# Optimization experiments

Measured on AMD Instinct MI355X. Metric: run time of the kernel, lower is better.

The kernel has to match this reference:

```python
import jax, jax.numpy as jnp
import numpy as np

B, S, DM, H = 2, 2048, 512, 8
DH = DM // H


def setup_inputs() -> dict:
    key = jax.random.key(0)
    ks = jax.random.split(key, 20)
    sc = 0.02
    d = {}
    d["q"] = jax.random.normal(ks[0], (B, S, DM), jnp.float32)
    d["k"] = jax.random.normal(ks[1], (B, S, DM), jnp.float32)
    d["v"] = jax.random.normal(ks[2], (B, S, DM), jnp.float32)
    d["xdiff"] = jax.random.normal(ks[3], (B, S, S), jnp.float32)
    d["mask"] = jax.random.randint(ks[4], (B, 1, 1, S), 0, 2, jnp.int32)
    # learned params (keras Dense: kernel + bias)
    d["Wq"] = jax.random.normal(ks[5], (DM, DM), jnp.float32) * sc
    d["bq"] = jnp.zeros((DM,), jnp.float32)
    d["Wk"] = jax.random.normal(ks[6], (DM, DM), jnp.float32) * sc
    d["bk"] = jnp.zeros((DM,), jnp.float32)
    d["Wv"] = jax.random.normal(ks[7], (DM, DM), jnp.float32) * sc
    d["bv"] = jnp.zeros((DM,), jnp.float32)
    d["Wa"] = jax.random.normal(ks[8], (DM, H), jnp.float32) * sc
    d["ba"] = jnp.zeros((H,), jnp.float32)
    d["Wb"] = jax.random.normal(ks[9], (DM, H), jnp.float32) * sc
    d["bb"] = jnp.zeros((H,), jnp.float32)
    d["Wo"] = jax.random.normal(ks[10], (DM, DM), jnp.float32) * sc
    d["bo"] = jnp.zeros((DM,), jnp.float32)
    return d


def reference(q, k, v, xdiff, mask, Wq, bq, Wk, bk, Wv, bv, Wa, ba, Wb, bb, Wo, bo):
    b, s, dm = q.shape
    h, dh = H, DH
    qp = q @ Wq + bq            # [B,S,DM]
    kp = k @ Wk + bk
    vp = v @ Wv + bv
    # per-head alpha/beta from projected q: [B,S,H] -> [B,H,S]
    a = jnp.transpose(qp @ Wa + ba, (0, 2, 1))
    bb_ = jnp.transpose(qp @ Wb + bb, (0, 2, 1))
    # split heads -> [B,H,S,DH]
    qh = qp.reshape(b, s, h, dh).transpose(0, 2, 1, 3)
    kh = kp.reshape(b, s, h, dh).transpose(0, 2, 1, 3)
    vh = vp.reshape(b, s, h, dh).transpose(0, 2, 1, 3)
    logits = jnp.einsum('bhqd,bhkd->bhqk', qh, kh) / jnp.sqrt(jnp.float32(dh))
    logits = logits + mask.astype(jnp.float32) * (-1e9)
    xd = xdiff[:, None]          # [B,1,S,S] broadcast over heads
    logits = logits + a[..., None] * xd + bb_[..., None] * (xd * xd)
    attn = jax.nn.softmax(logits, axis=-1)
    out = jnp.einsum('bhqk,bhkd->bhqd', attn, vh)
    out = out.transpose(0, 2, 1, 3).reshape(b, s, dm)
    return out @ Wo + bo, attn
```

## Files before the change

kernel.cpp:

```cpp
#include <hip/hip_runtime.h>
#include <stdint.h>

#define BB 2
#define SS 2048
#define DMODEL 512
#define NH 8
#define DHD 64

typedef __attribute__((ext_vector_type(8))) short bf16x8;
typedef __attribute__((ext_vector_type(4))) short s16x4;
typedef __attribute__((ext_vector_type(4))) float fx4;

__device__ __forceinline__ short f2bf(float f) {
    union { float f; uint32_t u; } c; c.f = f;
    uint32_t u = c.u;
    u += 0x7fffu + ((u >> 16) & 1u);
    return (short)(u >> 16);
}
__device__ __forceinline__ float bf2f(short s) {
    union { uint32_t u; float f; } c; c.u = ((uint32_t)(uint16_t)s) << 16;
    return c.f;
}

template<int A_BF16, int OUT_BF16>
__global__ __launch_bounds__(256, 4) void gemm_bias_k(
    const void* __restrict__ Ap, const float* __restrict__ W,
    const float* __restrict__ bias, void* __restrict__ Cp)
{
    __shared__ short As[64 * 40];
    __shared__ short Bs[64 * 40];
    const int tid = threadIdx.x;
    const int w = tid >> 6, lane = tid & 63;
    const int cl = lane & 15, quad = lane >> 4;
    const int mi = w >> 1, ni = w & 1;
    const int m0 = blockIdx.x * 64, n0 = blockIdx.y * 64;
    const float* Af = (const float*)Ap;
    const short* Ab = (const short*)Ap;
    fx4 acc[2][2] = {};

    for (int k0 = 0; k0 < DMODEL; k0 += 32) {
#pragma unroll
        for (int it = 0; it < 2; ++it) {
            int idx = tid + it * 256;
            int row = idx >> 3, kq = (idx & 7) * 4;
            s16x4 sv;
            if (A_BF16) {
                sv = *(const s16x4*)&Ab[(size_t)(m0 + row) * DMODEL + k0 + kq];
            } else {
                const float4 vv = *(const float4*)&Af[(size_t)(m0 + row) * DMODEL + k0 + kq];
                sv.x = f2bf(vv.x); sv.y = f2bf(vv.y); sv.z = f2bf(vv.z); sv.w = f2bf(vv.w);
            }
            *(s16x4*)&As[row * 40 + kq] = sv;
        }
#pragma unroll
        for (int it = 0; it < 2; ++it) {
            int idx = tid + it * 256;
            int kk = idx >> 4, nq = (idx & 15) * 4;
            const float4 vv = *(const float4*)&W[(size_t)(k0 + kk) * DMODEL + n0 + nq];
            Bs[(nq + 0) * 40 + kk] = f2bf(vv.x);
            Bs[(nq + 1) * 40 + kk] = f2bf(vv.y);
            Bs[(nq + 2) * 40 + kk] = f2bf(vv.z);
            Bs[(nq + 3) * 40 + kk] = f2bf(vv.w);
        }
        __syncthreads();
        bf16x8 af[2], bfr[2];
#pragma unroll
        for (int i = 0; i < 2; ++i)
            af[i] = *(const bf16x8*)&As[(mi * 32 + i * 16 + cl) * 40 + quad * 8];
#pragma unroll
        for (int j = 0; j < 2; ++j)
            bfr[j] = *(const bf16x8*)&Bs[(ni * 32 + j * 16 + cl) * 40 + quad * 8];
#pragma unroll
        for (int i = 0; i < 2; ++i)
#pragma unroll
            for (int j = 0; j < 2; ++j)
                acc[i][j] = __builtin_amdgcn_mfma_f32_16x16x32_bf16(af[i], bfr[j], acc[i][j], 0, 0, 0);
        __syncthreads();
    }
#pragma unroll
    for (int i = 0; i < 2; ++i) {
#pragma unroll
        for (int j = 0; j < 2; ++j) {
            int col = n0 + ni * 32 + j * 16 + cl;
            float bv = bias[col];
#pragma unroll
            for (int r = 0; r < 4; ++r) {
                int row = m0 + mi * 32 + i * 16 + quad * 4 + r;
                float v = acc[i][j][r] + bv;
                if (OUT_BF16) ((short*)Cp)[(size_t)row * DMODEL + col] = f2bf(v);
                else          ((float*)Cp)[(size_t)row * DMODEL + col] = v;
            }
        }
    }
}

__global__ __launch_bounds__(64) void ab_k(
    const short* __restrict__ qp,
    const float* __restrict__ Wa, const float* __restrict__ ba,
    const float* __restrict__ Wb, const float* __restrict__ bbias,
    float* __restrict__ a_ws, float* __restrict__ b_ws)
{
    const int r = blockIdx.x;
    const int b = r >> 11, s = r & 2047;
    const int lane = threadIdx.x;
    float qv[8];
    s16x4 q0 = *(const s16x4*)&qp[(size_t)r * DMODEL + lane * 8];
    s16x4 q1 = *(const s16x4*)&qp[(size_t)r * DMODEL + lane * 8 + 4];
    qv[0] = bf2f(q0.x); qv[1] = bf2f(q0.y); qv[2] = bf2f(q0.z); qv[3] = bf2f(q0.w);
    qv[4] = bf2f(q1.x); qv[5] = bf2f(q1.y); qv[6] = bf2f(q1.z); qv[7] = bf2f(q1.w);
    float pa[8] = {}, pb[8] = {};
#pragma unroll
    for (int kk = 0; kk < 8; ++kk) {
        int k = lane * 8 + kk;
        const float4 wa0 = *(const float4*)&Wa[k * 8];
        const float4 wa1 = *(const float4*)&Wa[k * 8 + 4];
        const float4 wb0 = *(const float4*)&Wb[k * 8];
        const float4 wb1 = *(const float4*)&Wb[k * 8 + 4];
        float qk = qv[kk];
        pa[0] += qk * wa0.x; pa[1] += qk * wa0.y; pa[2] += qk * wa0.z; pa[3] += qk * wa0.w;
        pa[4] += qk * wa1.x; pa[5] += qk * wa1.y; pa[6] += qk * wa1.z; pa[7] += qk * wa1.w;
        pb[0] += qk * wb0.x; pb[1] += qk * wb0.y; pb[2] += qk * wb0.z; pb[3] += qk * wb0.w;
        pb[4] += qk * wb1.x; pb[5] += qk * wb1.y; pb[6] += qk * wb1.z; pb[7] += qk * wb1.w;
    }
#pragma unroll
    for (int h = 0; h < 8; ++h) {
#pragma unroll
        for (int off = 1; off < 64; off <<= 1) {
            pa[h] += __shfl_xor(pa[h], off);
            pb[h] += __shfl_xor(pb[h], off);
        }
    }
    if (lane == 0) {
#pragma unroll
        for (int h = 0; h < 8; ++h) {
            a_ws[(b * NH + h) * SS + s] = pa[h] + ba[h];
            b_ws[(b * NH + h) * SS + s] = pb[h] + bbias[h];
        }
    }
}

__global__ __launch_bounds__(256, 2) void attn_k(
    const short* __restrict__ qp, const short* __restrict__ kp, const short* __restrict__ vp,
    const float* __restrict__ a_ws, const float* __restrict__ b_ws,
    const float* __restrict__ xdiff, const int* __restrict__ mask,
    float* __restrict__ attn, short* __restrict__ ao)
{
    __shared__ short qs[16 * 72];
    __shared__ short kv[4][64 * 72];
    __shared__ short ps[4][16 * 72];
    __shared__ float redm[64], reds[64], rowa[16], rowb[16];

    const int tid = threadIdx.x;
    const int w = tid >> 6, lane = tid & 63;
    const int cl = lane & 15, quad = lane >> 4;
    const int bh = blockIdx.x;
    const int b = bh >> 3, h = bh & 7;
    const int q0 = blockIdx.y * 16;
    const int bS = b * SS;

    for (int idx = tid; idx < 16 * 64; idx += 256) {
        int i = idx >> 6, k = idx & 63;
        qs[i * 72 + k] = qp[(size_t)(bS + q0 + i) * DMODEL + h * DHD + k];
    }
    if (tid < 16) {
        rowa[tid] = a_ws[(b * NH + h) * SS + q0 + tid];
        rowb[tid] = b_ws[(b * NH + h) * SS + q0 + tid];
    }
    __syncthreads();

    bf16x8 qf[2];
#pragma unroll
    for (int kc = 0; kc < 2; ++kc)
        qf[kc] = *(const bf16x8*)&qs[cl * 72 + kc * 32 + quad * 8];
    float ra[4], rb[4];
#pragma unroll
    for (int r = 0; r < 4; ++r) { ra[r] = rowa[quad * 4 + r]; rb[r] = rowb[quad * 4 + r]; }

    short* kvw = kv[w];
    short* psw = ps[w];
    const int j0w = w * 512;

    fx4 s[8][4];
    float rmax[4] = {-3e38f, -3e38f, -3e38f, -3e38f};

#pragma unroll
    for (int t = 0; t < 8; ++t) {
        const int j0 = j0w + t * 64;
#pragma unroll
        for (int p = 0; p < 16; ++p) {
            int jr = quad + p * 4;
            *(s16x4*)&kvw[jr * 72 + cl * 4] =
                *(const s16x4*)&kp[(size_t)(bS + j0 + jr) * DMODEL + h * DHD + cl * 4];
        }
        fx4 qk[4] = {};
#pragma unroll
        for (int nb = 0; nb < 4; ++nb)
#pragma unroll
            for (int kc = 0; kc < 2; ++kc) {
                bf16x8 kf = *(const bf16x8*)&kvw[(nb * 16 + cl) * 72 + kc * 32 + quad * 8];
                qk[nb] = __builtin_amdgcn_mfma_f32_16x16x32_bf16(qf[kc], kf, qk[nb], 0, 0, 0);
            }
#pragma unroll
        for (int nb = 0; nb < 4; ++nb) {
            const int j = j0 + nb * 16 + cl;
            const float mv = -1.0e9f * (float)mask[bS + j];
#pragma unroll
            for (int r = 0; r < 4; ++r) {
                const int qi = q0 + quad * 4 + r;
                const float xd = xdiff[(size_t)(bS + qi) * SS + j];
                float v = qk[nb][r] * 0.125f + mv + ra[r] * xd + rb[r] * (xd * xd);
                s[t][nb][r] = v;
                rmax[r] = fmaxf(rmax[r], v);
            }
        }
    }

#pragma unroll
    for (int off = 1; off < 16; off <<= 1)
#pragma unroll
        for (int r = 0; r < 4; ++r)
            rmax[r] = fmaxf(rmax[r], __shfl_xor(rmax[r], off));
    if (cl == 0)
#pragma unroll
        for (int r = 0; r < 4; ++r) redm[w * 16 + quad * 4 + r] = rmax[r];
    __syncthreads();
    float gm[4];
#pragma unroll
    for (int r = 0; r < 4; ++r) {
        int i = quad * 4 + r;
        gm[r] = fmaxf(fmaxf(redm[i], redm[16 + i]), fmaxf(redm[32 + i], redm[48 + i]));
    }

    float rsum[4] = {};
#pragma unroll
    for (int t = 0; t < 8; ++t)
#pragma unroll
        for (int nb = 0; nb < 4; ++nb)
#pragma unroll
            for (int r = 0; r < 4; ++r) {
                float e = exp2f((s[t][nb][r] - gm[r]) * 1.44269504f);
                s[t][nb][r] = e;
                rsum[r] += e;
            }
#pragma unroll
    for (int off = 1; off < 16; off <<= 1)
#pragma unroll
        for (int r = 0; r < 4; ++r)
            rsum[r] += __shfl_xor(rsum[r], off);
    if (cl == 0)
#pragma unroll
        for (int r = 0; r < 4; ++r) reds[w * 16 + quad * 4 + r] = rsum[r];
    __syncthreads();
    float gs[4];
#pragma unroll
    for (int r = 0; r < 4; ++r) {
        int i = quad * 4 + r;
        gs[r] = 1.0f / (reds[i] + reds[16 + i] + reds[32 + i] + reds[48 + i]);
    }

    fx4 oacc[4] = {};
    float* attn_bh = attn + (size_t)(b * NH + h) * SS * SS;
#pragma unroll
    for (int t = 0; t < 8; ++t) {
        const int j0 = j0w + t * 64;
#pragma unroll
        for (int p4 = 0; p4 < 16; ++p4) {
            s16x4 tmp;
            tmp.x = vp[(size_t)(bS + j0 + p4 * 4 + 0) * DMODEL + h * DHD + lane];
            tmp.y = vp[(size_t)(bS + j0 + p4 * 4 + 1) * DMODEL + h * DHD + lane];
            tmp.z = vp[(size_t)(bS + j0 + p4 * 4 + 2) * DMODEL + h * DHD + lane];
            tmp.w = vp[(size_t)(bS + j0 + p4 * 4 + 3) * DMODEL + h * DHD + lane];
            *(s16x4*)&kvw[lane * 72 + p4 * 4] = tmp;
        }
#pragma unroll
        for (int nb = 0; nb < 4; ++nb) {
            const int j = j0 + nb * 16 + cl;
#pragma unroll
            for (int r = 0; r < 4; ++r) {
                float p = s[t][nb][r] * gs[r];
                attn_bh[(size_t)(q0 + quad * 4 + r) * SS + j] = p;
                psw[(quad * 4 + r) * 72 + nb * 16 + cl] = f2bf(p);
            }
        }
        bf16x8 pf[2];
#pragma unroll
        for (int kc = 0; kc < 2; ++kc)
            pf[kc] = *(const bf16x8*)&psw[cl * 72 + kc * 32 + quad * 8];
#pragma unroll
        for (int nb = 0; nb < 4; ++nb)
#pragma unroll
            for (int kc = 0; kc < 2; ++kc) {
                bf16x8 vf = *(const bf16x8*)&kvw[(nb * 16 + cl) * 72 + kc * 32 + quad * 8];
                oacc[nb] = __builtin_amdgcn_mfma_f32_16x16x32_bf16(pf[kc], vf, oacc[nb], 0, 0, 0);
            }
    }

    __syncthreads();
    float* ored = (float*)kv;
#pragma unroll
    for (int nb = 0; nb < 4; ++nb)
#pragma unroll
        for (int r = 0; r < 4; ++r)
            ored[w * 1024 + (quad * 4 + r) * 64 + nb * 16 + cl] = oacc[nb][r];
    __syncthreads();
    {
        int i = tid >> 4, dq = (tid & 15) * 4;
        float sx = 0, sy = 0, sz = 0, sw = 0;
#pragma unroll
        for (int ww = 0; ww < 4; ++ww) {
            const float4 vv = *(const float4*)&ored[ww * 1024 + i * 64 + dq];
            sx += vv.x; sy += vv.y; sz += vv.z; sw += vv.w;
        }
        s16x4 o;
        o.x = f2bf(sx); o.y = f2bf(sy); o.z = f2bf(sz); o.w = f2bf(sw);
        *(s16x4*)&ao[(size_t)(bS + q0 + i) * DMODEL + h * DHD + dq] = o;
    }
}

extern "C" void kernel_launch(void* const* d_in, const int* in_sizes, int n_in,
                              void* d_out, int out_size, void* d_ws, size_t ws_size,
                              hipStream_t stream)
{
    (void)in_sizes; (void)n_in; (void)out_size; (void)ws_size;
    const float* q     = (const float*)d_in[0];
    const float* k     = (const float*)d_in[1];
    const float* v     = (const float*)d_in[2];
    const float* xdiff = (const float*)d_in[3];
    const int*   mask  = (const int*)d_in[4];
    const float* Wq = (const float*)d_in[5];
    const float* bq = (const float*)d_in[6];
    const float* Wk = (const float*)d_in[7];
    const float* bk = (const float*)d_in[8];
    const float* Wv = (const float*)d_in[9];
    const float* bv = (const float*)d_in[10];
    const float* Wa = (const float*)d_in[11];
    const float* ba = (const float*)d_in[12];
    const float* Wb = (const float*)d_in[13];
    const float* bb = (const float*)d_in[14];
    const float* Wo = (const float*)d_in[15];
    const float* bo = (const float*)d_in[16];

    char* ws = (char*)d_ws;
    short* qp   = (short*)(ws + 0);
    short* kp   = (short*)(ws + 4194304);
    short* vp   = (short*)(ws + 8388608);
    float* a_ws = (float*)(ws + 12582912);
    float* b_ws = (float*)(ws + 12713984);
    short* ao   = (short*)(ws + 12845056);

    float* out  = (float*)d_out;
    float* attn = out + (size_t)BB * SS * DMODEL;

    dim3 g(64, 8), blk(256);
    hipLaunchKernelGGL((gemm_bias_k<0, 1>), g, blk, 0, stream, q, Wq, bq, qp);
    hipLaunchKernelGGL((gemm_bias_k<0, 1>), g, blk, 0, stream, k, Wk, bk, kp);
    hipLaunchKernelGGL((gemm_bias_k<0, 1>), g, blk, 0, stream, v, Wv, bv, vp);
    hipLaunchKernelGGL(ab_k, dim3(4096), dim3(64), 0, stream, qp, Wa, ba, Wb, bb, a_ws, b_ws);
    hipLaunchKernelGGL(attn_k, dim3(16, 128), dim3(256), 0, stream,
                       qp, kp, vp, a_ws, b_ws, xdiff, mask, attn, ao);
    hipLaunchKernelGGL((gemm_bias_k<1, 0>), g, blk, 0, stream, ao, Wo, bo, out);
}
```

Before: 546.7 us.

## Fuse QKV projections, store V transposed, widen attention to 8 waves

The three input projection GEMMs become one launch over a z-dimension, and the V projection is written transposed as [B, DM, S]. The attention kernel then reads K and transposed V fragments straight from global memory instead of staging them through LDS. It also doubles the block to 512 threads (8 waves, 256 keys each), which halves the per-wave score register array. The cost of the uncoalesced strided V gathers and per-tile LDS copies is meant to go away, in exchange for scattered 8-byte transposed stores in the V GEMM and more reliance on L2 for K/V reuse.

```diff
diff --git a/kernel.cpp b/kernel.cpp
--- a/kernel.cpp
+++ b/kernel.cpp
@@ -22,10 +22,11 @@
     return c.f;
 }
 
-template<int A_BF16, int OUT_BF16>
-__global__ __launch_bounds__(256, 4) void gemm_bias_k(
-    const void* __restrict__ Ap, const float* __restrict__ W,
-    const float* __restrict__ bias, void* __restrict__ Cp)
+__global__ __launch_bounds__(256, 4) void qkv_gemm_k(
+    const float* __restrict__ q, const float* __restrict__ Wq, const float* __restrict__ bq,
+    const float* __restrict__ k, const float* __restrict__ Wk, const float* __restrict__ bk,
+    const float* __restrict__ v, const float* __restrict__ Wv, const float* __restrict__ bv,
+    short* __restrict__ qp, short* __restrict__ kp, short* __restrict__ vt)
 {
     __shared__ short As[64 * 40];
     __shared__ short Bs[64 * 40];
@@ -34,8 +35,10 @@
     const int cl = lane & 15, quad = lane >> 4;
     const int mi = w >> 1, ni = w & 1;
     const int m0 = blockIdx.x * 64, n0 = blockIdx.y * 64;
-    const float* Af = (const float*)Ap;
-    const short* Ab = (const short*)Ap;
+    const int z = blockIdx.z;
+    const float* Af   = (z == 0) ? q  : (z == 1) ? k  : v;
+    const float* W    = (z == 0) ? Wq : (z == 1) ? Wk : Wv;
+    const float* bias = (z == 0) ? bq : (z == 1) ? bk : bv;
     fx4 acc[2][2] = {};
 
     for (int k0 = 0; k0 < DMODEL; k0 += 32) {
@@ -43,13 +46,9 @@
         for (int it = 0; it < 2; ++it) {
             int idx = tid + it * 256;
             int row = idx >> 3, kq = (idx & 7) * 4;
+            const float4 vv = *(const float4*)&Af[(size_t)(m0 + row) * DMODEL + k0 + kq];
             s16x4 sv;
-            if (A_BF16) {
-                sv = *(const s16x4*)&Ab[(size_t)(m0 + row) * DMODEL + k0 + kq];
-            } else {
-                const float4 vv = *(const float4*)&Af[(size_t)(m0 + row) * DMODEL + k0 + kq];
-                sv.x = f2bf(vv.x); sv.y = f2bf(vv.y); sv.z = f2bf(vv.z); sv.w = f2bf(vv.w);
-            }
+            sv.x = f2bf(vv.x); sv.y = f2bf(vv.y); sv.z = f2bf(vv.z); sv.w = f2bf(vv.w);
             *(s16x4*)&As[row * 40 + kq] = sv;
         }
 #pragma unroll
@@ -77,21 +76,89 @@
                 acc[i][j] = __builtin_amdgcn_mfma_f32_16x16x32_bf16(af[i], bfr[j], acc[i][j], 0, 0, 0);
         __syncthreads();
     }
+    short* Cp = (z == 0) ? qp : (z == 1) ? kp : vt;
 #pragma unroll
     for (int i = 0; i < 2; ++i) {
 #pragma unroll
         for (int j = 0; j < 2; ++j) {
             int col = n0 + ni * 32 + j * 16 + cl;
-            float bv = bias[col];
+            float bv4 = bias[col];
+            int rowbase = m0 + mi * 32 + i * 16 + quad * 4;
+            if (z < 2) {
+#pragma unroll
+                for (int r = 0; r < 4; ++r)
+                    Cp[(size_t)(rowbase + r) * DMODEL + col] = f2bf(acc[i][j][r] + bv4);
+            } else {
+                int b = rowbase >> 11, s0 = rowbase & 2047;
+                s16x4 o;
+                o.x = f2bf(acc[i][j][0] + bv4);
+                o.y = f2bf(acc[i][j][1] + bv4);
+                o.z = f2bf(acc[i][j][2] + bv4);
+                o.w = f2bf(acc[i][j][3] + bv4);
+                *(s16x4*)&Cp[((size_t)b * DMODEL + col) * SS + s0] = o;
+            }
+        }
+    }
+}
+
+__global__ __launch_bounds__(256, 4) void out_gemm_k(
+    const short* __restrict__ Ab, const float* __restrict__ W,
+    const float* __restrict__ bias, float* __restrict__ Cp)
+{
+    __shared__ short As[64 * 40];
+    __shared__ short Bs[64 * 40];
+    const int tid = threadIdx.x;
+    const int w = tid >> 6, lane = tid & 63;
+    const int cl = lane & 15, quad = lane >> 4;
+    const int mi = w >> 1, ni = w & 1;
+    const int m0 = blockIdx.x * 64, n0 = blockIdx.y * 64;
+    fx4 acc[2][2] = {};
+
+    for (int k0 = 0; k0 < DMODEL; k0 += 32) {
+#pragma unroll
+        for (int it = 0; it < 2; ++it) {
+            int idx = tid + it * 256;
+            int row = idx >> 3, kq = (idx & 7) * 4;
+            *(s16x4*)&As[row * 40 + kq] =
+                *(const s16x4*)&Ab[(size_t)(m0 + row) * DMODEL + k0 + kq];
+        }
+#pragma unroll
+        for (int it = 0; it < 2; ++it) {
+            int idx = tid + it * 256;
+            int kk = idx >> 4, nq = (idx & 15) * 4;
+            const float4 vv = *(const float4*)&W[(size_t)(k0 + kk) * DMODEL + n0 + nq];
+            Bs[(nq + 0) * 40 + kk] = f2bf(vv.x);
+            Bs[(nq + 1) * 40 + kk] = f2bf(vv.y);
+            Bs[(nq + 2) * 40 + kk] = f2bf(vv.z);
+            Bs[(nq + 3) * 40 + kk] = f2bf(vv.w);
+        }
+        __syncthreads();
+        bf16x8 af[2], bfr[2];
+#pragma unroll
+        for (int i = 0; i < 2; ++i)
+            af[i] = *(const bf16x8*)&As[(mi * 32 + i * 16 + cl) * 40 + quad * 8];
+#pragma unroll
+        for (int j = 0; j < 2; ++j)
+            bfr[j] = *(const bf16x8*)&Bs[(ni * 32 + j * 16 + cl) * 40 + quad * 8];
+#pragma unroll
+        for (int i = 0; i < 2; ++i)
+#pragma unroll
+            for (int j = 0; j < 2; ++j)
+                acc[i][j] = __builtin_amdgcn_mfma_f32_16x16x32_bf16(af[i], bfr[j], acc[i][j], 0, 0, 0);
+        __syncthreads();
+    }
+#pragma unroll
+    for (int i = 0; i < 2; ++i)
+#pragma unroll
+        for (int j = 0; j < 2; ++j) {
+            int col = n0 + ni * 32 + j * 16 + cl;
+            float bv4 = bias[col];
 #pragma unroll
             for (int r = 0; r < 4; ++r) {
                 int row = m0 + mi * 32 + i * 16 + quad * 4 + r;
-                float v = acc[i][j][r] + bv;
-                if (OUT_BF16) ((short*)Cp)[(size_t)row * DMODEL + col] = f2bf(v);
-                else          ((float*)Cp)[(size_t)row * DMODEL + col] = v;
-            }
-        }
-    }
+                Cp[(size_t)row * DMODEL + col] = acc[i][j][r] + bv4;
+            }
+        }
 }
 
 __global__ __launch_bounds__(64) void ab_k(
@@ -101,7 +168,6 @@
     float* __restrict__ a_ws, float* __restrict__ b_ws)
 {
     const int r = blockIdx.x;
-    const int b = r >> 11, s = r & 2047;
     const int lane = threadIdx.x;
     float qv[8];
     s16x4 q0 = *(const s16x4*)&qp[(size_t)r * DMODEL + lane * 8];
@@ -123,14 +189,14 @@
         pb[4] += qk * wb1.x; pb[5] += qk * wb1.y; pb[6] += qk * wb1.z; pb[7] += qk * wb1.w;
     }
 #pragma unroll
-    for (int h = 0; h < 8; ++h) {
+    for (int h = 0; h < 8; ++h)
 #pragma unroll
         for (int off = 1; off < 64; off <<= 1) {
             pa[h] += __shfl_xor(pa[h], off);
             pb[h] += __shfl_xor(pb[h], off);
         }
-    }
     if (lane == 0) {
+        int b = r >> 11, s = r & 2047;
 #pragma unroll
         for (int h = 0; h < 8; ++h) {
             a_ws[(b * NH + h) * SS + s] = pa[h] + ba[h];
@@ -139,16 +205,15 @@
     }
 }
 
-__global__ __launch_bounds__(256, 2) void attn_k(
-    const short* __restrict__ qp, const short* __restrict__ kp, const short* __restrict__ vp,
+__global__ __launch_bounds__(512, 4) void attn_k(
+    const short* __restrict__ qp, const short* __restrict__ kp, const short* __restrict__ vt,
     const float* __restrict__ a_ws, const float* __restrict__ b_ws,
     const float* __restrict__ xdiff, const int* __restrict__ mask,
     float* __restrict__ attn, short* __restrict__ ao)
 {
-    __shared__ short qs[16 * 72];
-    __shared__ short kv[4][64 * 72];
-    __shared__ short ps[4][16 * 72];
-    __shared__ float redm[64], reds[64], rowa[16], rowb[16];
+    __shared__ short ps[8][16 * 72];
+    __shared__ float ored[4][16 * 68];
+    __shared__ float redm[128], reds[128], rowa[16], rowb[16];
 
     const int tid = threadIdx.x;
     const int w = tid >> 6, lane = tid & 63;
@@ -158,59 +223,49 @@
     const int q0 = blockIdx.y * 16;
     const int bS = b * SS;
 
-    for (int idx = tid; idx < 16 * 64; idx += 256) {
-        int i = idx >> 6, k = idx & 63;
-        qs[i * 72 + k] = qp[(size_t)(bS + q0 + i) * DMODEL + h * DHD + k];
-    }
     if (tid < 16) {
-        rowa[tid] = a_ws[(b * NH + h) * SS + q0 + tid];
-        rowb[tid] = b_ws[(b * NH + h) * SS + q0 + tid];
-    }
-    __syncthreads();
-
+        rowa[tid] = a_ws[bh * SS + q0 + tid];
+        rowb[tid] = b_ws[bh * SS + q0 + tid];
+    }
+    __syncthreads();
+
+    const short* qbase = qp + (size_t)(bS + q0 + cl) * DMODEL + h * DHD + quad * 8;
     bf16x8 qf[2];
-#pragma unroll
-    for (int kc = 0; kc < 2; ++kc)
-        qf[kc] = *(const bf16x8*)&qs[cl * 72 + kc * 32 + quad * 8];
+    qf[0] = *(const bf16x8*)(qbase);
+    qf[1] = *(const bf16x8*)(qbase + 32);
+
     float ra[4], rb[4];
 #pragma unroll
     for (int r = 0; r < 4; ++r) { ra[r] = rowa[quad * 4 + r]; rb[r] = rowb[quad * 4 + r]; }
 
-    short* kvw = kv[w];
-    short* psw = ps[w];
-    const int j0w = w * 512;
-
-    fx4 s[8][4];
+    const int j0w = w * 256;
+    fx4 s[4][4];
     float rmax[4] = {-3e38f, -3e38f, -3e38f, -3e38f};
 
 #pragma unroll
-    for (int t = 0; t < 8; ++t) {
+    for (int t = 0; t < 4; ++t) {
         const int j0 = j0w + t * 64;
-#pragma unroll
-        for (int p = 0; p < 16; ++p) {
-            int jr = quad + p * 4;
-            *(s16x4*)&kvw[jr * 72 + cl * 4] =
-                *(const s16x4*)&kp[(size_t)(bS + j0 + jr) * DMODEL + h * DHD + cl * 4];
-        }
         fx4 qk[4] = {};
 #pragma unroll
-        for (int nb = 0; nb < 4; ++nb)
+        for (int nb = 0; nb < 4; ++nb) {
+            const short* kb = kp + (size_t)(bS + j0 + nb * 16 + cl) * DMODEL + h * DHD + quad * 8;
 #pragma unroll
             for (int kc = 0; kc < 2; ++kc) {
-                bf16x8 kf = *(const bf16x8*)&kvw[(nb * 16 + cl) * 72 + kc * 32 + quad * 8];
+                bf16x8 kf = *(const bf16x8*)(kb + kc * 32);
                 qk[nb] = __builtin_amdgcn_mfma_f32_16x16x32_bf16(qf[kc], kf, qk[nb], 0, 0, 0);
             }
+        }
 #pragma unroll
         for (int nb = 0; nb < 4; ++nb) {
             const int j = j0 + nb * 16 + cl;
             const float mv = -1.0e9f * (float)mask[bS + j];
+            const float* xrow = xdiff + (size_t)(bS + q0 + quad * 4) * SS + j;
 #pragma unroll
             for (int r = 0; r < 4; ++r) {
-                const int qi = q0 + quad * 4 + r;
-                const float xd = xdiff[(size_t)(bS + qi) * SS + j];
-                float v = qk[nb][r] * 0.125f + mv + ra[r] * xd + rb[r] * (xd * xd);
-                s[t][nb][r] = v;
-                rmax[r] = fmaxf(rmax[r], v);
+                const float xd = xrow[(size_t)r * SS];
+                float val = qk[nb][r] * 0.125f + mv + ra[r] * xd + rb[r] * (xd * xd);
+                s[t][nb][r] = val;
+                rmax[r] = fmaxf(rmax[r], val);
             }
         }
     }
@@ -228,17 +283,21 @@
 #pragma unroll
     for (int r = 0; r < 4; ++r) {
         int i = quad * 4 + r;
-        gm[r] = fmaxf(fmaxf(redm[i], redm[16 + i]), fmaxf(redm[32 + i], redm[48 + i]));
+        float m01 = fmaxf(redm[i], redm[16 + i]);
+        float m23 = fmaxf(redm[32 + i], redm[48 + i]);
+        float m45 = fmaxf(redm[64 + i], redm[80 + i]);
+        float m67 = fmaxf(redm[96 + i], redm[112 + i]);
+        gm[r] = fmaxf(fmaxf(m01, m23), fmaxf(m45, m67));
     }
 
     float rsum[4] = {};
 #pragma unroll
-    for (int t = 0; t < 8; ++t)
+    for (int t = 0; t < 4; ++t)
 #pragma unroll
         for (int nb = 0; nb < 4; ++nb)
 #pragma unroll
             for (int r = 0; r < 4; ++r) {
-                float e = exp2f((s[t][nb][r] - gm[r]) * 1.44269504f);
+                float e = __builtin_amdgcn_exp2f((s[t][nb][r] - gm[r]) * 1.44269504f);
                 s[t][nb][r] = e;
                 rsum[r] += e;
             }
@@ -255,60 +314,67 @@
 #pragma unroll
     for (int r = 0; r < 4; ++r) {
         int i = quad * 4 + r;
-        gs[r] = 1.0f / (reds[i] + reds[16 + i] + reds[32 + i] + reds[48 + i]);
+        float s0 = reds[i] + reds[16 + i] + reds[32 + i] + reds[48 + i];
+        float s1 = reds[64 + i] + reds[80 + i] + reds[96 + i] + reds[112 + i];
+        gs[r] = 1.0f / (s0 + s1);
     }
 
     fx4 oacc[4] = {};
-    float* attn_bh = attn + (size_t)(b * NH + h) * SS * SS;
-#pragma unroll
-    for (int t = 0; t < 8; ++t) {
+    float* attn_bh = attn + (size_t)bh * SS * SS;
+    short* psw = ps[w];
+    const short* vtb = vt + ((size_t)b * DMODEL + h * DHD) * SS;
+#pragma unroll
+    for (int t = 0; t < 4; ++t) {
         const int j0 = j0w + t * 64;
-#pragma unroll
-        for (int p4 = 0; p4 < 16; ++p4) {
-            s16x4 tmp;
-            tmp.x = vp[(size_t)(bS + j0 + p4 * 4 + 0) * DMODEL + h * DHD + lane];
-            tmp.y = vp[(size_t)(bS + j0 + p4 * 4 + 1) * DMODEL + h * DHD + lane];
-            tmp.z = vp[(size_t)(bS + j0 + p4 * 4 + 2) * DMODEL + h * DHD + lane];
-            tmp.w = vp[(size_t)(bS + j0 + p4 * 4 + 3) * DMODEL + h * DHD + lane];
-            *(s16x4*)&kvw[lane * 72 + p4 * 4] = tmp;
-        }
 #pragma unroll
         for (int nb = 0; nb < 4; ++nb) {
             const int j = j0 + nb * 16 + cl;
+            float* arow = attn_bh + (size_t)(q0 + quad * 4) * SS + j;
 #pragma unroll
             for (int r = 0; r < 4; ++r) {
                 float p = s[t][nb][r] * gs[r];
-                attn_bh[(size_t)(q0 + quad * 4 + r) * SS + j] = p;
+                arow[(size_t)r * SS] = p;
                 psw[(quad * 4 + r) * 72 + nb * 16 + cl] = f2bf(p);
             }
         }
         bf16x8 pf[2];
-#pragma unroll
-        for (int kc = 0; kc < 2; ++kc)
-            pf[kc] = *(const bf16x8*)&psw[cl * 72 + kc * 32 + quad * 8];
+        pf[0] = *(const bf16x8*)&psw[cl * 72 + quad * 8];
+        pf[1] = *(const bf16x8*)&psw[cl * 72 + 32 + quad * 8];
+#pragma unroll
+        for (int nb = 0; nb < 4; ++nb) {
+            const short* vb = vtb + (size_t)(nb * 16 + cl) * SS + j0 + quad * 8;
+#pragma unroll
+            for (int kc = 0; kc < 2; ++kc) {
+                bf16x8 vf = *(const bf16x8*)(vb + kc * 32);
+                oacc[nb] = __builtin_amdgcn_mfma_f32_16x16x32_bf16(pf[kc], vf, oacc[nb], 0, 0, 0);
+            }
+        }
+    }
+
+    __syncthreads();
+    if (w < 4) {
 #pragma unroll
         for (int nb = 0; nb < 4; ++nb)
 #pragma unroll
-            for (int kc = 0; kc < 2; ++kc) {
-                bf16x8 vf = *(const bf16x8*)&kvw[(nb * 16 + cl) * 72 + kc * 32 + quad * 8];
-                oacc[nb] = __builtin_amdgcn_mfma_f32_16x16x32_bf16(pf[kc], vf, oacc[nb], 0, 0, 0);
-            }
-    }
-
-    __syncthreads();
-    float* ored = (float*)kv;
-#pragma unroll
-    for (int nb = 0; nb < 4; ++nb)
-#pragma unroll
-        for (int r = 0; r < 4; ++r)
-            ored[w * 1024 + (quad * 4 + r) * 64 + nb * 16 + cl] = oacc[nb][r];
-    __syncthreads();
-    {
+            for (int r = 0; r < 4; ++r)
+                ored[w][(quad * 4 + r) * 68 + nb * 16 + cl] = oacc[nb][r];
+    }
+    __syncthreads();
+    if (w >= 4) {
+        float* o = ored[w - 4];
+#pragma unroll
+        for (int nb = 0; nb < 4; ++nb)
+#pragma unroll
+            for (int r = 0; r < 4; ++r)
+                o[(quad * 4 + r) * 68 + nb * 16 + cl] += oacc[nb][r];
+    }
+    __syncthreads();
+    if (tid < 256) {
         int i = tid >> 4, dq = (tid & 15) * 4;
         float sx = 0, sy = 0, sz = 0, sw = 0;
 #pragma unroll
         for (int ww = 0; ww < 4; ++ww) {
-            const float4 vv = *(const float4*)&ored[ww * 1024 + i * 64 + dq];
+            const float4 vv = *(const float4*)&ored[ww][i * 68 + dq];
             sx += vv.x; sy += vv.y; sz += vv.z; sw += vv.w;
         }
         s16x4 o;
@@ -343,7 +409,7 @@
     char* ws = (char*)d_ws;
     short* qp   = (short*)(ws + 0);
     short* kp   = (short*)(ws + 4194304);
-    short* vp   = (short*)(ws + 8388608);
+    short* vt   = (short*)(ws + 8388608);
     float* a_ws = (float*)(ws + 12582912);
     float* b_ws = (float*)(ws + 12713984);
     short* ao   = (short*)(ws + 12845056);
@@ -351,12 +417,10 @@
     float* out  = (float*)d_out;
     float* attn = out + (size_t)BB * SS * DMODEL;
 
-    dim3 g(64, 8), blk(256);
-    hipLaunchKernelGGL((gemm_bias_k<0, 1>), g, blk, 0, stream, q, Wq, bq, qp);
-    hipLaunchKernelGGL((gemm_bias_k<0, 1>), g, blk, 0, stream, k, Wk, bk, kp);
-    hipLaunchKernelGGL((gemm_bias_k<0, 1>), g, blk, 0, stream, v, Wv, bv, vp);
+    hipLaunchKernelGGL(qkv_gemm_k, dim3(64, 8, 3), dim3(256), 0, stream,
+                       q, Wq, bq, k, Wk, bk, v, Wv, bv, qp, kp, vt);
     hipLaunchKernelGGL(ab_k, dim3(4096), dim3(64), 0, stream, qp, Wa, ba, Wb, bb, a_ws, b_ws);
-    hipLaunchKernelGGL(attn_k, dim3(16, 128), dim3(256), 0, stream,
-                       qp, kp, vp, a_ws, b_ws, xdiff, mask, attn, ao);
-    hipLaunchKernelGGL((gemm_bias_k<1, 0>), g, blk, 0, stream, ao, Wo, bo, out);
-}
+    hipLaunchKernelGGL(attn_k, dim3(16, 128), dim3(512), 0, stream,
+                       qp, kp, vt, a_ws, b_ws, xdiff, mask, attn, ao);
+    hipLaunchKernelGGL(out_gemm_k, dim3(64, 8), dim3(256), 0, stream, ao, Wo, bo, out);
+}
```

Measured after the change: 547.5 us. No clear change (+0.1%).
